# Performance work log

Measured on AMD Instinct MI355X. Metric: run time of the kernel, lower is better.

The kernel has to match this reference:

```python
import jax, jax.numpy as jnp
import numpy as np

QUERY_INDS = (0, 1, 2, 3)
HEADS = 8
HEAD_DIM = 64
SCALE = HEAD_DIM ** -0.5
DIM = 512
INNER = HEADS * HEAD_DIM  # 512


def setup_inputs() -> dict:
    key = jax.random.key(0)
    ks = jax.random.split(key, 6)
    B, N = 4, 2048
    x = jax.random.normal(ks[0], (B, N, DIM), dtype=jnp.float32)
    bias = jax.random.normal(ks[1], (B, HEADS, N, N), dtype=jnp.float32)
    # weights stored as (in, out); math-equivalent to torch Linear
    Wq = jax.random.normal(ks[2], (DIM, INNER), dtype=jnp.float32) * (DIM ** -0.5)
    Wkv = jax.random.normal(ks[3], (DIM, 2 * INNER), dtype=jnp.float32) * (DIM ** -0.5)
    Wo = jax.random.normal(ks[4], (INNER, DIM), dtype=jnp.float32) * (INNER ** -0.5)
    bo = jax.random.normal(ks[5], (DIM,), dtype=jnp.float32) * 0.01
    return {"x": x, "bias": bias, "Wq": Wq, "Wkv": Wkv, "Wo": Wo, "bo": bo}


def _split_heads(t):
    # (B, n, H*d) -> (B, H, n, d)
    B, n, _ = t.shape
    return t.reshape(B, n, HEADS, HEAD_DIM).transpose(0, 2, 1, 3)


def reference(x, bias, Wq, Wkv, Wo, bo):
    qi = jnp.array(QUERY_INDS)
    q = _split_heads(x[:, qi] @ Wq)          # (B, H, M, d), M = len(QUERY_INDS)
    kv = x @ Wkv                              # (B, N, 2*inner)
    k, v = jnp.split(kv, 2, axis=-1)
    k = _split_heads(k)                       # (B, H, N, d)
    v = _split_heads(v)                       # (B, H, N, d)
    dots = jnp.einsum('bhmd,bhnd->bhmn', q, k) * SCALE
    dots = dots + bias[:, :, qi]              # gather bias rows at query positions
    attn = jax.nn.softmax(dots, axis=-1)      # dropout=0 (eval)
    out = jnp.einsum('bhmn,bhnd->bhmd', attn, v)
    B, _, M, _ = out.shape
    out = out.transpose(0, 2, 1, 3).reshape(B, M, INNER)  # (B, M, H*d)
    return out @ Wo + bo
```

## Files before the change

### kernel.cpp

```cpp
#include <hip/hip_runtime.h>
#include <stddef.h>

#define B_ 4
#define N_ 2048
#define C_ 512
#define H_ 8
#define D_ 64
#define M_ 4
#define HM_ 32
#define S_ 64
#define SCALE_ 0.125f

#define QK_OFF   0
#define PAX_OFF  65536
#define MLOC_OFF (65536 + 4194304)
#define LLOC_OFF (MLOC_OFF + 8192)
#define QP_OFF   (LLOC_OFF + 8192)
#define OVP_OFF  (QP_OFF + 65536)

__global__ __launch_bounds__(256) void k1a_q(const float* __restrict__ x, const float* __restrict__ Wq,
                                             float* __restrict__ q_part) {
    __shared__ float W[64][68];
    __shared__ float xr[16][68];
    int t = threadIdx.x;
    int c0 = blockIdx.x * 64, j0 = blockIdx.y * 64;
    #pragma unroll
    for (int i = 0; i < 4; i++) {
        int f = t + i * 256; int cc = f >> 4, j4 = f & 15;
        *(float4*)&W[cc][j4 * 4] = *(const float4*)&Wq[(size_t)(c0 + cc) * 512 + j0 + j4 * 4];
    }
    {
        int r = t >> 4, c4 = t & 15;
        int b = r >> 2, m = r & 3;
        *(float4*)&xr[r][c4 * 4] = *(const float4*)&x[((size_t)(b * N_) + m) * C_ + c0 + c4 * 4];
    }
    __syncthreads();
    int j = t & 63, rg = t >> 6;
    float acc[4] = {0, 0, 0, 0};
    #pragma unroll 16
    for (int cc = 0; cc < 64; cc++) {
        float w = W[cc][j];
        #pragma unroll
        for (int i = 0; i < 4; i++) acc[i] += xr[rg * 4 + i][cc] * w;
    }
    #pragma unroll
    for (int i = 0; i < 4; i++) {
        int r = rg * 4 + i;
        q_part[((size_t)blockIdx.x * 16 + r) * 512 + j0 + j] = acc[i];
    }
}

__global__ __launch_bounds__(256) void k1b_qk(const float* __restrict__ Wkv, const float* __restrict__ q_part,
                                              float* __restrict__ qk_ws, float* __restrict__ out) {
    __shared__ float WkT[64][68];
    __shared__ float qh[16][68];
    int t = threadIdx.x;
    int c0 = blockIdx.x * 64; int h = blockIdx.y;
    int bid = blockIdx.y * 8 + blockIdx.x;
    if (bid < 32) out[bid * 256 + t] = 0.f;
    #pragma unroll
    for (int i = 0; i < 4; i++) {
        int f = t + i * 256; int cc = f >> 4, d4 = f & 15;
        float4 v = *(const float4*)&Wkv[(size_t)(c0 + cc) * 1024 + h * 64 + d4 * 4];
        WkT[d4 * 4 + 0][cc] = v.x; WkT[d4 * 4 + 1][cc] = v.y;
        WkT[d4 * 4 + 2][cc] = v.z; WkT[d4 * 4 + 3][cc] = v.w;
    }
    {
        int r = t >> 4, d4 = t & 15;
        float4 a = make_float4(0.f, 0.f, 0.f, 0.f);
        #pragma unroll
        for (int cs = 0; cs < 8; cs++) {
            float4 v = *(const float4*)&q_part[((size_t)cs * 16 + r) * 512 + h * 64 + d4 * 4];
            a.x += v.x; a.y += v.y; a.z += v.z; a.w += v.w;
        }
        *(float4*)&qh[r][d4 * 4] = a;
    }
    __syncthreads();
    int c = t & 63, rg = t >> 6;
    float acc[4] = {0, 0, 0, 0};
    #pragma unroll 16
    for (int d = 0; d < 64; d++) {
        float w = WkT[d][c];
        #pragma unroll
        for (int i = 0; i < 4; i++) acc[i] += qh[rg * 4 + i][d] * w;
    }
    #pragma unroll
    for (int i = 0; i < 4; i++) {
        int r = rg * 4 + i; int b = r >> 2, m = r & 3;
        qk_ws[((size_t)(b * HM_) + h * M_ + m) * 512 + c0 + c] = acc[i] * SCALE_;
    }
}

__global__ __launch_bounds__(256) void k234_flash(const float* __restrict__ x, const float* __restrict__ qk_ws,
                                                  const float* __restrict__ bias,
                                                  float* __restrict__ pax, float* __restrict__ mloc,
                                                  float* __restrict__ lloc) {
    __shared__ __align__(16) float qk_s[32][516];
    __shared__ __align__(16) float scratch[4][32][32];
    __shared__ __align__(16) float dmat[32][36];
    __shared__ __align__(16) float pT[32][36];
    __shared__ float mrow[32];
    __shared__ float red8[32][8];
    int t = threadIdx.x;
    int s = blockIdx.x, b = blockIdx.y;
    int n0 = s * 32;

    #pragma unroll
    for (int k = 0; k < 16; k++) {
        int idx = t + k * 256;
        int row = idx >> 7, c4 = idx & 127;
        *(float4*)&qk_s[row][c4 * 4] =
            *(const float4*)&qk_ws[((size_t)(b * HM_) + row) * 512 + c4 * 4];
    }
    __syncthreads();

    int hmg = t >> 6;
    int ng  = (t >> 3) & 7;
    int cs  = t & 7;
    float d[8][4];
    #pragma unroll
    for (int i = 0; i < 8; i++)
        #pragma unroll
        for (int jn = 0; jn < 4; jn++) d[i][jn] = 0.f;

    const float* xp = &x[((size_t)(b * N_) + n0 + ng * 4) * C_];
    const float* qrow = &qk_s[hmg * 8][0];
    #pragma unroll 2
    for (int step = 0; step < 16; step++) {
        int cbase = cs * 4 + step * 32;
        float4 xv[4];
        #pragma unroll
        for (int jn = 0; jn < 4; jn++)
            xv[jn] = *(const float4*)&xp[(size_t)jn * C_ + cbase];
        #pragma unroll
        for (int i = 0; i < 8; i++) {
            float4 qv = *(const float4*)&qrow[i * 516 + cbase];
            #pragma unroll
            for (int jn = 0; jn < 4; jn++) {
                d[i][jn] += qv.x * xv[jn].x + qv.y * xv[jn].y + qv.z * xv[jn].z + qv.w * xv[jn].w;
            }
        }
    }
    int pos = hmg * 8 + ng;
    if (cs >= 4) {
        #pragma unroll
        for (int i = 0; i < 8; i++)
            *(float4*)&scratch[cs - 4][pos][i * 4] = make_float4(d[i][0], d[i][1], d[i][2], d[i][3]);
    }
    __syncthreads();
    if (cs < 4) {
        #pragma unroll
        for (int i = 0; i < 8; i++) {
            float4 v = *(float4*)&scratch[cs][pos][i * 4];
            d[i][0] += v.x; d[i][1] += v.y; d[i][2] += v.z; d[i][3] += v.w;
        }
    }
    __syncthreads();
    if (cs == 2 || cs == 3) {
        #pragma unroll
        for (int i = 0; i < 8; i++)
            *(float4*)&scratch[cs - 2][pos][i * 4] = make_float4(d[i][0], d[i][1], d[i][2], d[i][3]);
    }
    __syncthreads();
    if (cs < 2) {
        #pragma unroll
        for (int i = 0; i < 8; i++) {
            float4 v = *(float4*)&scratch[cs][pos][i * 4];
            d[i][0] += v.x; d[i][1] += v.y; d[i][2] += v.z; d[i][3] += v.w;
        }
    }
    __syncthreads();
    if (cs == 1) {
        #pragma unroll
        for (int i = 0; i < 8; i++)
            *(float4*)&scratch[0][pos][i * 4] = make_float4(d[i][0], d[i][1], d[i][2], d[i][3]);
    }
    __syncthreads();
    if (cs == 0) {
        #pragma unroll
        for (int i = 0; i < 8; i++) {
            float4 v = *(float4*)&scratch[0][pos][i * 4];
            *(float4*)&dmat[hmg * 8 + i][ng * 4] =
                make_float4(d[i][0] + v.x, d[i][1] + v.y, d[i][2] + v.z, d[i][3] + v.w);
        }
    }
    __syncthreads();

    int row = t >> 3, j = t & 7;
    int h = row >> 2, m = row & 3;
    float4 dv = *(float4*)&dmat[row][j * 4];
    float4 bv = *(const float4*)&bias[(((size_t)(b * H_) + h) * N_ + m) * N_ + n0 + j * 4];
    float v0 = dv.x + bv.x, v1 = dv.y + bv.y, v2 = dv.z + bv.z, v3 = dv.w + bv.w;
    float pmax = fmaxf(fmaxf(v0, v1), fmaxf(v2, v3));
    red8[row][j] = pmax;
    __syncthreads();
    if (j == 0) {
        float mg = red8[row][0];
        #pragma unroll
        for (int k = 1; k < 8; k++) mg = fmaxf(mg, red8[row][k]);
        mrow[row] = mg;
    }
    __syncthreads();
    float mg = mrow[row];
    float e0 = __expf(v0 - mg), e1 = __expf(v1 - mg), e2 = __expf(v2 - mg), e3 = __expf(v3 - mg);
    red8[row][j] = e0 + e1 + e2 + e3;
    __syncthreads();
    if (j == 0) {
        float ls = red8[row][0];
        #pragma unroll
        for (int k = 1; k < 8; k++) ls += red8[row][k];
        mloc[((size_t)(s * B_) + b) * HM_ + row] = mg;
        lloc[((size_t)(s * B_) + b) * HM_ + row] = ls;
    }
    pT[j * 4 + 0][row] = e0; pT[j * 4 + 1][row] = e1;
    pT[j * 4 + 2][row] = e2; pT[j * 4 + 3][row] = e3;
    __syncthreads();

    int cg = t & 63, hw = t >> 6;
    float o[8][8];
    #pragma unroll
    for (int i = 0; i < 8; i++)
        #pragma unroll
        for (int jj = 0; jj < 8; jj++) o[i][jj] = 0.f;
    const float* xb = &x[((size_t)(b * N_) + n0) * C_];
    #pragma unroll 4
    for (int n = 0; n < 32; n++) {
        float4 pa = *(float4*)&pT[n][hw * 8];
        float4 pb = *(float4*)&pT[n][hw * 8 + 4];
        float4 xa = *(const float4*)&xb[(size_t)n * C_ + cg * 4];
        float4 xc = *(const float4*)&xb[(size_t)n * C_ + 256 + cg * 4];
        float pv[8] = {pa.x, pa.y, pa.z, pa.w, pb.x, pb.y, pb.z, pb.w};
        #pragma unroll
        for (int i = 0; i < 8; i++) {
            o[i][0] += pv[i] * xa.x; o[i][1] += pv[i] * xa.y;
            o[i][2] += pv[i] * xa.z; o[i][3] += pv[i] * xa.w;
            o[i][4] += pv[i] * xc.x; o[i][5] += pv[i] * xc.y;
            o[i][6] += pv[i] * xc.z; o[i][7] += pv[i] * xc.w;
        }
    }
    #pragma unroll
    for (int i = 0; i < 8; i++) {
        int hm = hw * 8 + i;
        float* dst = &pax[(((size_t)(s * B_) + b) * HM_ + hm) * 512];
        *(float4*)&dst[cg * 4]       = make_float4(o[i][0], o[i][1], o[i][2], o[i][3]);
        *(float4*)&dst[256 + cg * 4] = make_float4(o[i][4], o[i][5], o[i][6], o[i][7]);
    }
}

__global__ __launch_bounds__(256) void k5a_ov(const float* __restrict__ Wkv, const float* __restrict__ pax,
                                              const float* __restrict__ mloc, const float* __restrict__ lloc,
                                              float* __restrict__ ov_part) {
    __shared__ float Wv[64][68];
    __shared__ float axh[16][68];
    __shared__ float sc[64][16];
    __shared__ float redm[16][16];
    __shared__ float mgl[16], lgl[16];
    int t = threadIdx.x;
    int c0 = blockIdx.x * 64; int h = blockIdx.y;
    #pragma unroll
    for (int i = 0; i < 4; i++) {
        int f = t + i * 256; int cc = f >> 4, e4 = f & 15;
        *(float4*)&Wv[cc][e4 * 4] =
            *(const float4*)&Wkv[(size_t)(c0 + cc) * 1024 + 512 + h * 64 + e4 * 4];
    }
    int r = t & 15, sg = t >> 4;
    int b = r >> 2, m = r & 3;
    float pm = -1e30f;
    #pragma unroll
    for (int k = 0; k < 4; k++) {
        int s = sg * 4 + k;
        pm = fmaxf(pm, mloc[((size_t)(s * B_) + b) * HM_ + h * M_ + m]);
    }
    redm[sg][r] = pm;
    __syncthreads();
    if (t < 16) {
        float mg = redm[0][t];
        #pragma unroll
        for (int k = 1; k < 16; k++) mg = fmaxf(mg, redm[k][t]);
        mgl[t] = mg;
    }
    __syncthreads();
    float mg = mgl[r];
    float pl = 0.f;
    #pragma unroll
    for (int k = 0; k < 4; k++) {
        int s = sg * 4 + k;
        float w = __expf(mloc[((size_t)(s * B_) + b) * HM_ + h * M_ + m] - mg);
        sc[s][r] = w;
        pl += w * lloc[((size_t)(s * B_) + b) * HM_ + h * M_ + m];
    }
    redm[sg][r] = pl;
    __syncthreads();
    if (t < 16) {
        float l = redm[0][t];
        #pragma unroll
        for (int k = 1; k < 16; k++) l += redm[k][t];
        lgl[t] = 1.0f / l;
    }
    __syncthreads();
    float inv = lgl[r];
    #pragma unroll
    for (int k = 0; k < 4; k++) sc[sg * 4 + k][r] *= inv;
    __syncthreads();
    {
        int rr = t >> 4, c4 = t & 15;
        int bb = rr >> 2, mm = rr & 3;
        float4 a = make_float4(0.f, 0.f, 0.f, 0.f);
        for (int s = 0; s < 64; s++) {
            float w = sc[s][rr];
            float4 v = *(const float4*)&pax[(((size_t)(s * B_) + bb) * HM_ + h * M_ + mm) * 512 + c0 + c4 * 4];
            a.x += w * v.x; a.y += w * v.y; a.z += w * v.z; a.w += w * v.w;
        }
        *(float4*)&axh[rr][c4 * 4] = a;
    }
    __syncthreads();
    int e = t & 63, rg = t >> 6;
    float acc[4] = {0, 0, 0, 0};
    #pragma unroll 16
    for (int cc = 0; cc < 64; cc++) {
        float w = Wv[cc][e];
        #pragma unroll
        for (int i = 0; i < 4; i++) acc[i] += axh[rg * 4 + i][cc] * w;
    }
    #pragma unroll
    for (int i = 0; i < 4; i++) {
        int rr = rg * 4 + i;
        ov_part[((size_t)blockIdx.x * 16 + rr) * 512 + h * 64 + e] = acc[i];
    }
}

__global__ __launch_bounds__(256) void k5b_out(const float* __restrict__ Wo, const float* __restrict__ bo,
                                               const float* __restrict__ ov_part, float* __restrict__ out) {
    __shared__ float W[64][68];
    __shared__ float ovr[16][68];
    int t = threadIdx.x;
    int i0 = blockIdx.x * 64; int j0 = blockIdx.y * 64;
    #pragma unroll
    for (int i = 0; i < 4; i++) {
        int f = t + i * 256; int ii = f >> 4, j4 = f & 15;
        *(float4*)&W[ii][j4 * 4] = *(const float4*)&Wo[(size_t)(i0 + ii) * 512 + j0 + j4 * 4];
    }
    {
        int r = t >> 4, c4 = t & 15;
        float4 a = make_float4(0.f, 0.f, 0.f, 0.f);
        #pragma unroll
        for (int cs = 0; cs < 8; cs++) {
            float4 v = *(const float4*)&ov_part[((size_t)cs * 16 + r) * 512 + i0 + c4 * 4];
            a.x += v.x; a.y += v.y; a.z += v.z; a.w += v.w;
        }
        *(float4*)&ovr[r][c4 * 4] = a;
    }
    __syncthreads();
    int j = t & 63, rg = t >> 6;
    float binit = (blockIdx.x == 0) ? bo[j0 + j] : 0.f;
    float acc[4] = {binit, binit, binit, binit};
    #pragma unroll 16
    for (int ii = 0; ii < 64; ii++) {
        float w = W[ii][j];
        #pragma unroll
        for (int i = 0; i < 4; i++) acc[i] += ovr[rg * 4 + i][ii] * w;
    }
    #pragma unroll
    for (int i = 0; i < 4; i++) {
        int r = rg * 4 + i;
        atomicAdd(&out[r * 512 + j0 + j], acc[i]);
    }
}

extern "C" void kernel_launch(void* const* d_in, const int* in_sizes, int n_in,
                              void* d_out, int out_size, void* d_ws, size_t ws_size,
                              hipStream_t stream) {
    const float* x    = (const float*)d_in[0];
    const float* bias = (const float*)d_in[1];
    const float* Wq   = (const float*)d_in[2];
    const float* Wkv  = (const float*)d_in[3];
    const float* Wo   = (const float*)d_in[4];
    const float* bo   = (const float*)d_in[5];
    float* out = (float*)d_out;
    float* ws  = (float*)d_ws;

    float* qk_ws   = ws + QK_OFF;
    float* pax     = ws + PAX_OFF;
    float* mloc    = ws + MLOC_OFF;
    float* lloc    = ws + LLOC_OFF;
    float* q_part  = ws + QP_OFF;
    float* ov_part = ws + OVP_OFF;

    k1a_q<<<dim3(8, 8), 256, 0, stream>>>(x, Wq, q_part);
    k1b_qk<<<dim3(8, 8), 256, 0, stream>>>(Wkv, q_part, qk_ws, out);
    k234_flash<<<dim3(S_, B_), 256, 0, stream>>>(x, qk_ws, bias, pax, mloc, lloc);
    k5a_ov<<<dim3(8, 8), 256, 0, stream>>>(Wkv, pax, mloc, lloc, ov_part);
    k5b_out<<<dim3(8, 8), 256, 0, stream>>>(Wo, bo, ov_part, out);
}
```

Baseline: 610.1 us.

## Fuse Q projection into QK kernel, shuffle-reduce dots, split OV over slices

Merges the two Q-projection kernels into one, where each block recomputes its head's Q over all input channels. This removes one launch and the q_part round trip through global memory. The flash kernel's cross-thread partial-sum reduction now uses wavefront xor-shuffles instead of several shared-memory passes and barriers. The OV kernel gains a z-dimension that splits the 64 sequence chunks into 4 groups for more parallelism, and the output kernel sums 32 partial slices instead of 8. The trade-off is redundant Q compute per block and a larger partial buffer to reduce.

Result: slower. 627.6 us (+2.9%).

```diff
diff --git a/kernel.cpp b/kernel.cpp
--- a/kernel.cpp
+++ b/kernel.cpp
@@ -15,72 +15,57 @@
 #define PAX_OFF  65536
 #define MLOC_OFF (65536 + 4194304)
 #define LLOC_OFF (MLOC_OFF + 8192)
-#define QP_OFF   (LLOC_OFF + 8192)
-#define OVP_OFF  (QP_OFF + 65536)
-
-__global__ __launch_bounds__(256) void k1a_q(const float* __restrict__ x, const float* __restrict__ Wq,
-                                             float* __restrict__ q_part) {
+#define OVP_OFF  (LLOC_OFF + 8192)
+
+__global__ __launch_bounds__(256) void k1_qk(const float* __restrict__ x, const float* __restrict__ Wq,
+                                             const float* __restrict__ Wkv,
+                                             float* __restrict__ qk_ws, float* __restrict__ out) {
     __shared__ float W[64][68];
     __shared__ float xr[16][68];
-    int t = threadIdx.x;
-    int c0 = blockIdx.x * 64, j0 = blockIdx.y * 64;
-    #pragma unroll
-    for (int i = 0; i < 4; i++) {
-        int f = t + i * 256; int cc = f >> 4, j4 = f & 15;
-        *(float4*)&W[cc][j4 * 4] = *(const float4*)&Wq[(size_t)(c0 + cc) * 512 + j0 + j4 * 4];
-    }
-    {
-        int r = t >> 4, c4 = t & 15;
-        int b = r >> 2, m = r & 3;
-        *(float4*)&xr[r][c4 * 4] = *(const float4*)&x[((size_t)(b * N_) + m) * C_ + c0 + c4 * 4];
-    }
-    __syncthreads();
-    int j = t & 63, rg = t >> 6;
-    float acc[4] = {0, 0, 0, 0};
-    #pragma unroll 16
-    for (int cc = 0; cc < 64; cc++) {
-        float w = W[cc][j];
-        #pragma unroll
-        for (int i = 0; i < 4; i++) acc[i] += xr[rg * 4 + i][cc] * w;
-    }
-    #pragma unroll
-    for (int i = 0; i < 4; i++) {
-        int r = rg * 4 + i;
-        q_part[((size_t)blockIdx.x * 16 + r) * 512 + j0 + j] = acc[i];
-    }
-}
-
-__global__ __launch_bounds__(256) void k1b_qk(const float* __restrict__ Wkv, const float* __restrict__ q_part,
-                                              float* __restrict__ qk_ws, float* __restrict__ out) {
-    __shared__ float WkT[64][68];
     __shared__ float qh[16][68];
     int t = threadIdx.x;
     int c0 = blockIdx.x * 64; int h = blockIdx.y;
     int bid = blockIdx.y * 8 + blockIdx.x;
     if (bid < 32) out[bid * 256 + t] = 0.f;
+
+    int j = t & 63, rg = t >> 6;
+    float qacc[4] = {0, 0, 0, 0};
+    for (int ch = 0; ch < 8; ch++) {
+        int cc0 = ch * 64;
+        #pragma unroll
+        for (int i = 0; i < 4; i++) {
+            int f = t + i * 256; int cc = f >> 4, j4 = f & 15;
+            *(float4*)&W[cc][j4 * 4] = *(const float4*)&Wq[(size_t)(cc0 + cc) * 512 + h * 64 + j4 * 4];
+        }
+        {
+            int r = t >> 4, c4 = t & 15;
+            int b = r >> 2, m = r & 3;
+            *(float4*)&xr[r][c4 * 4] = *(const float4*)&x[((size_t)(b * N_) + m) * C_ + cc0 + c4 * 4];
+        }
+        __syncthreads();
+        #pragma unroll 16
+        for (int cc = 0; cc < 64; cc++) {
+            float w = W[cc][j];
+            #pragma unroll
+            for (int i = 0; i < 4; i++) qacc[i] += xr[rg * 4 + i][cc] * w;
+        }
+        __syncthreads();
+    }
+    #pragma unroll
+    for (int i = 0; i < 4; i++) qh[rg * 4 + i][j] = qacc[i];
     #pragma unroll
     for (int i = 0; i < 4; i++) {
         int f = t + i * 256; int cc = f >> 4, d4 = f & 15;
         float4 v = *(const float4*)&Wkv[(size_t)(c0 + cc) * 1024 + h * 64 + d4 * 4];
-        WkT[d4 * 4 + 0][cc] = v.x; WkT[d4 * 4 + 1][cc] = v.y;
-        WkT[d4 * 4 + 2][cc] = v.z; WkT[d4 * 4 + 3][cc] = v.w;
-    }
-    {
-        int r = t >> 4, d4 = t & 15;
-        float4 a = make_float4(0.f, 0.f, 0.f, 0.f);
-        #pragma unroll
-        for (int cs = 0; cs < 8; cs++) {
-            float4 v = *(const float4*)&q_part[((size_t)cs * 16 + r) * 512 + h * 64 + d4 * 4];
-            a.x += v.x; a.y += v.y; a.z += v.z; a.w += v.w;
-        }
-        *(float4*)&qh[r][d4 * 4] = a;
-    }
-    __syncthreads();
-    int c = t & 63, rg = t >> 6;
+        W[d4 * 4 + 0][cc] = v.x; W[d4 * 4 + 1][cc] = v.y;
+        W[d4 * 4 + 2][cc] = v.z; W[d4 * 4 + 3][cc] = v.w;
+    }
+    __syncthreads();
+    int c = j;
     float acc[4] = {0, 0, 0, 0};
     #pragma unroll 16
     for (int d = 0; d < 64; d++) {
-        float w = WkT[d][c];
+        float w = W[d][c];
         #pragma unroll
         for (int i = 0; i < 4; i++) acc[i] += qh[rg * 4 + i][d] * w;
     }
@@ -96,7 +81,6 @@
                                                   float* __restrict__ pax, float* __restrict__ mloc,
                                                   float* __restrict__ lloc) {
     __shared__ __align__(16) float qk_s[32][516];
-    __shared__ __align__(16) float scratch[4][32][32];
     __shared__ __align__(16) float dmat[32][36];
     __shared__ __align__(16) float pT[32][36];
     __shared__ float mrow[32];
@@ -141,48 +125,19 @@
             }
         }
     }
-    int pos = hmg * 8 + ng;
-    if (cs >= 4) {
+    #pragma unroll
+    for (int i = 0; i < 8; i++) {
+        #pragma unroll
+        for (int jn = 0; jn < 4; jn++) {
+            d[i][jn] += __shfl_xor(d[i][jn], 1, 64);
+            d[i][jn] += __shfl_xor(d[i][jn], 2, 64);
+            d[i][jn] += __shfl_xor(d[i][jn], 4, 64);
+        }
+    }
+    if (cs == 0) {
         #pragma unroll
         for (int i = 0; i < 8; i++)
-            *(float4*)&scratch[cs - 4][pos][i * 4] = make_float4(d[i][0], d[i][1], d[i][2], d[i][3]);
-    }
-    __syncthreads();
-    if (cs < 4) {
-        #pragma unroll
-        for (int i = 0; i < 8; i++) {
-            float4 v = *(float4*)&scratch[cs][pos][i * 4];
-            d[i][0] += v.x; d[i][1] += v.y; d[i][2] += v.z; d[i][3] += v.w;
-        }
-    }
-    __syncthreads();
-    if (cs == 2 || cs == 3) {
-        #pragma unroll
-        for (int i = 0; i < 8; i++)
-            *(float4*)&scratch[cs - 2][pos][i * 4] = make_float4(d[i][0], d[i][1], d[i][2], d[i][3]);
-    }
-    __syncthreads();
-    if (cs < 2) {
-        #pragma unroll
-        for (int i = 0; i < 8; i++) {
-            float4 v = *(float4*)&scratch[cs][pos][i * 4];
-            d[i][0] += v.x; d[i][1] += v.y; d[i][2] += v.z; d[i][3] += v.w;
-        }
-    }
-    __syncthreads();
-    if (cs == 1) {
-        #pragma unroll
-        for (int i = 0; i < 8; i++)
-            *(float4*)&scratch[0][pos][i * 4] = make_float4(d[i][0], d[i][1], d[i][2], d[i][3]);
-    }
-    __syncthreads();
-    if (cs == 0) {
-        #pragma unroll
-        for (int i = 0; i < 8; i++) {
-            float4 v = *(float4*)&scratch[0][pos][i * 4];
-            *(float4*)&dmat[hmg * 8 + i][ng * 4] =
-                make_float4(d[i][0] + v.x, d[i][1] + v.y, d[i][2] + v.z, d[i][3] + v.w);
-        }
+            *(float4*)&dmat[hmg * 8 + i][ng * 4] = make_float4(d[i][0], d[i][1], d[i][2], d[i][3]);
     }
     __syncthreads();
 
@@ -256,7 +211,7 @@
     __shared__ float redm[16][16];
     __shared__ float mgl[16], lgl[16];
     int t = threadIdx.x;
-    int c0 = blockIdx.x * 64; int h = blockIdx.y;
+    int c0 = blockIdx.x * 64; int h = blockIdx.y; int z = blockIdx.z;
     #pragma unroll
     for (int i = 0; i < 4; i++) {
         int f = t + i * 256; int cc = f >> 4, e4 = f & 15;
@@ -274,18 +229,18 @@
     redm[sg][r] = pm;
     __syncthreads();
     if (t < 16) {
-        float mg = redm[0][t];
-        #pragma unroll
-        for (int k = 1; k < 16; k++) mg = fmaxf(mg, redm[k][t]);
-        mgl[t] = mg;
-    }
-    __syncthreads();
-    float mg = mgl[r];
+        float mgv = redm[0][t];
+        #pragma unroll
+        for (int k = 1; k < 16; k++) mgv = fmaxf(mgv, redm[k][t]);
+        mgl[t] = mgv;
+    }
+    __syncthreads();
+    float mgv = mgl[r];
     float pl = 0.f;
     #pragma unroll
     for (int k = 0; k < 4; k++) {
         int s = sg * 4 + k;
-        float w = __expf(mloc[((size_t)(s * B_) + b) * HM_ + h * M_ + m] - mg);
+        float w = __expf(mloc[((size_t)(s * B_) + b) * HM_ + h * M_ + m] - mgv);
         sc[s][r] = w;
         pl += w * lloc[((size_t)(s * B_) + b) * HM_ + h * M_ + m];
     }
@@ -306,7 +261,9 @@
         int rr = t >> 4, c4 = t & 15;
         int bb = rr >> 2, mm = rr & 3;
         float4 a = make_float4(0.f, 0.f, 0.f, 0.f);
-        for (int s = 0; s < 64; s++) {
+        #pragma unroll 8
+        for (int k = 0; k < 16; k++) {
+            int s = z * 16 + k;
             float w = sc[s][rr];
             float4 v = *(const float4*)&pax[(((size_t)(s * B_) + bb) * HM_ + h * M_ + mm) * 512 + c0 + c4 * 4];
             a.x += w * v.x; a.y += w * v.y; a.z += w * v.z; a.w += w * v.w;
@@ -322,10 +279,11 @@
         #pragma unroll
         for (int i = 0; i < 4; i++) acc[i] += axh[rg * 4 + i][cc] * w;
     }
+    int slice = z * 8 + blockIdx.x;
     #pragma unroll
     for (int i = 0; i < 4; i++) {
         int rr = rg * 4 + i;
-        ov_part[((size_t)blockIdx.x * 16 + rr) * 512 + h * 64 + e] = acc[i];
+        ov_part[((size_t)slice * 16 + rr) * 512 + h * 64 + e] = acc[i];
     }
 }
 
@@ -343,8 +301,8 @@
     {
         int r = t >> 4, c4 = t & 15;
         float4 a = make_float4(0.f, 0.f, 0.f, 0.f);
-        #pragma unroll
-        for (int cs = 0; cs < 8; cs++) {
+        #pragma unroll 8
+        for (int cs = 0; cs < 32; cs++) {
             float4 v = *(const float4*)&ov_part[((size_t)cs * 16 + r) * 512 + i0 + c4 * 4];
             a.x += v.x; a.y += v.y; a.z += v.z; a.w += v.w;
         }
@@ -370,6 +328,7 @@
 extern "C" void kernel_launch(void* const* d_in, const int* in_sizes, int n_in,
                               void* d_out, int out_size, void* d_ws, size_t ws_size,
                               hipStream_t stream) {
+    (void)in_sizes; (void)n_in; (void)out_size; (void)ws_size;
     const float* x    = (const float*)d_in[0];
     const float* bias = (const float*)d_in[1];
     const float* Wq   = (const float*)d_in[2];
@@ -383,12 +342,10 @@
     float* pax     = ws + PAX_OFF;
     float* mloc    = ws + MLOC_OFF;
     float* lloc    = ws + LLOC_OFF;
-    float* q_part  = ws + QP_OFF;
     float* ov_part = ws + OVP_OFF;
 
-    k1a_q<<<dim3(8, 8), 256, 0, stream>>>(x, Wq, q_part);
-    k1b_qk<<<dim3(8, 8), 256, 0, stream>>>(Wkv, q_part, qk_ws, out);
+    k1_qk<<<dim3(8, 8), 256, 0, stream>>>(x, Wq, Wkv, qk_ws, out);
     k234_flash<<<dim3(S_, B_), 256, 0, stream>>>(x, qk_ws, bias, pax, mloc, lloc);
-    k5a_ov<<<dim3(8, 8), 256, 0, stream>>>(Wkv, pax, mloc, lloc, ov_part);
+    k5a_ov<<<dim3(8, 8, 4), 256, 0, stream>>>(Wkv, pax, mloc, lloc, ov_part);
     k5b_out<<<dim3(8, 8), 256, 0, stream>>>(Wo, bo, ov_part, out);
 }
```
